# Performance work log

Hardware: AMD Instinct MI355X
Metric: run time of the kernel (lower is better)

Reference implementation:

```python
import jax, jax.numpy as jnp
import numpy as np

B, H, N, D, A = 96, 100, 128, 768, 256  # batch, max_history_num, news_num, news_embedding_dim, attention_dim


def setup_inputs() -> dict:
    key = jax.random.key(0)
    ks = jax.random.split(key, 6)
    w = lambda k, shape: jax.random.normal(k, shape, jnp.float32) * 0.02
    return {
        "history_embedding": jax.random.normal(ks[0], (B, H, D), jnp.float32),
        "candidate_news_representation": jax.random.normal(ks[1], (B, N, D), jnp.float32),
        "W_l": w(ks[2], (D, D)),              # SAGEConv lin_l (neighbor) weight
        "b_l": jnp.zeros((D,), jnp.float32),  # SAGEConv lin_l bias
        "W_r": w(ks[3], (D, D)),              # SAGEConv lin_r (root) weight, bias=False
        "W_K": w(ks[4], (A, D)),              # K Linear, bias=False
        "W_Q": w(ks[5], (A, D)),              # Q Linear, bias=True
        "b_Q": jnp.zeros((A,), jnp.float32),
    }


def reference(history_embedding, candidate_news_representation, W_l, b_l, W_r, W_K, W_Q, b_Q):
    b, h, d = history_embedding.shape
    n = candidate_news_representation.shape[1]
    a_dim = W_K.shape[0]

    # --- GraphSAGE (1 layer SAGEConv, mean aggr, PyG node_dim=-2) ---
    # edge_index: src = user rows 0..b-1 (indexing the history dim!), dst = 0..h-1.
    # Every dst h receives all srcs 0..b-1, so the mean-aggregated neighbor feature is
    # mean over the first b history slots, identical for every h.
    neigh = jnp.mean(history_embedding[:, :b, :], axis=1)  # [b, d]
    gcn = (
        jnp.einsum("bhd,ed->bhe", history_embedding, W_r)
        + (neigh @ W_l.T + b_l)[:, None, :]
    )  # [b, h, d]

    # --- K/Q attention pooling over history ---
    user_rep = gcn[:, 0, :]                                  # [b, d] (gcn_feature[:, :1, :])
    K = jnp.einsum("bhd,ad->bha", gcn, W_K)                  # [b, h, A]
    Q = user_rep @ W_Q.T + b_Q                               # [b, A]
    scores = jnp.einsum("bha,ba->bh", K, Q) / jnp.sqrt(jnp.float32(a_dim))
    alpha = jax.nn.softmax(scores, axis=1)                   # [b, h]
    out = jnp.einsum("bh,bhd->bd", alpha, gcn)               # [b, d]

    # In torch, news_rep/user_rep2 are expand()ed over news_num with identical content,
    # so the per-candidate outputs are all equal: broadcast instead of recomputing.
    return jnp.broadcast_to(out[:, None, :], (b, n, d))
```

## Files before the change

kernel.cpp:

```cpp
#include <hip/hip_runtime.h>
#include <hip/hip_bf16.h>

#define BB 96
#define HH 100
#define NN 128
#define DD 768
#define AA 256

#define WSLAB 196608
#define WSLAB4 49152

static __device__ __forceinline__ float dot4(float4 a, float4 b) {
  return a.x * b.x + a.y * b.y + a.z * b.z + a.w * b.w;
}

__global__ void __launch_bounds__(256)
k_prep(const float* __restrict__ Wr, const float* __restrict__ WK,
       const float* __restrict__ hist,
       float* __restrict__ MTp, float* __restrict__ neighp) {
  int bid = blockIdx.x, tid = threadIdx.x;
  if (bid < 768) {
    __shared__ float sL[32][33];
    __shared__ float sR[32][33];
    int s = bid / 192;
    int t = bid % 192;
    int d0 = (t % 24) * 32, a0 = (t / 24) * 32;
    int tx = tid & 31, ty = tid >> 5;
    float acc[4] = {0.f, 0.f, 0.f, 0.f};
    int ebase = s * 192;
    for (int e0 = ebase; e0 < ebase + 192; e0 += 32) {
#pragma unroll
      for (int k = 0; k < 4; ++k) {
        sL[ty + 8 * k][tx] = WK[(size_t)(a0 + ty + 8 * k) * DD + e0 + tx];
        sR[ty + 8 * k][tx] = Wr[(size_t)(e0 + ty + 8 * k) * DD + d0 + tx];
      }
      __syncthreads();
#pragma unroll 8
      for (int e = 0; e < 32; ++e) {
        float w = sR[e][tx];
#pragma unroll
        for (int k = 0; k < 4; ++k) acc[k] += sL[ty + 8 * k][e] * w;
      }
      __syncthreads();
    }
#pragma unroll
    for (int k = 0; k < 4; ++k) sL[ty + 8 * k][tx] = acc[k];
    __syncthreads();
    float* MTs = MTp + (size_t)s * WSLAB;
#pragma unroll
    for (int k = 0; k < 4; ++k)
      MTs[(size_t)(d0 + ty + 8 * k) * AA + a0 + tx] = sL[tx][ty + 8 * k];
  } else {
    int id = bid - 768;
    int b = id % BB, hg = id / BB;
    if (tid < 192) {
      const float* hb = hist + (size_t)b * HH * DD + (size_t)hg * 12 * DD + tid * 4;
      float4 acc = make_float4(0.f, 0.f, 0.f, 0.f);
#pragma unroll
      for (int i = 0; i < 12; ++i) {
        float4 x = *(const float4*)(hb + (size_t)i * DD);
        acc.x += x.x; acc.y += x.y; acc.z += x.z; acc.w += x.w;
      }
      *(float4*)(neighp + ((size_t)hg * BB + b) * DD + tid * 4) = acc;
    }
  }
}

__global__ void k_nl_u0(const float* __restrict__ neighp, const float* __restrict__ hist,
                        const float* __restrict__ Wl, const float* __restrict__ bl,
                        const float* __restrict__ Wr,
                        float* __restrict__ nl, float* __restrict__ u0) {
  int e0 = blockIdx.x * 32;
  int b0 = blockIdx.y * 3;
  int lane = threadIdx.x & 63, wave = threadIdx.x >> 6;
  float4 xn[3][3], xh[3][3];
#pragma unroll
  for (int bi = 0; bi < 3; ++bi) {
    int b = b0 + bi;
#pragma unroll
    for (int jj = 0; jj < 3; ++jj) {
      int idx = lane + 64 * jj;
      float4 s = make_float4(0.f, 0.f, 0.f, 0.f);
#pragma unroll
      for (int g = 0; g < 8; ++g) {
        float4 x = ((const float4*)(neighp + ((size_t)g * BB + b) * DD))[idx];
        s.x += x.x; s.y += x.y; s.z += x.z; s.w += x.w;
      }
      xn[bi][jj] = make_float4(s.x * (1.f / 96.f), s.y * (1.f / 96.f),
                               s.z * (1.f / 96.f), s.w * (1.f / 96.f));
      xh[bi][jj] = ((const float4*)(hist + (size_t)b * HH * DD))[idx];
    }
  }
  for (int i = 0; i < 8; ++i) {
    int e = e0 + wave * 8 + i;
    const float4* wl4 = (const float4*)(Wl + (size_t)e * DD);
    const float4* wr4 = (const float4*)(Wr + (size_t)e * DD);
    float pl[3] = {0.f, 0.f, 0.f}, pr[3] = {0.f, 0.f, 0.f};
#pragma unroll
    for (int jj = 0; jj < 3; ++jj) {
      float4 wl = wl4[lane + 64 * jj];
      float4 wr = wr4[lane + 64 * jj];
#pragma unroll
      for (int bi = 0; bi < 3; ++bi) {
        pl[bi] += dot4(wl, xn[bi][jj]);
        pr[bi] += dot4(wr, xh[bi][jj]);
      }
    }
#pragma unroll
    for (int bi = 0; bi < 3; ++bi) {
      float pp = pl[bi], qq = pr[bi];
      for (int off = 32; off; off >>= 1) {
        pp += __shfl_down(pp, off, 64);
        qq += __shfl_down(qq, off, 64);
      }
      if (lane == 0) {
        float nle = pp + bl[e];
        nl[(size_t)(b0 + bi) * DD + e] = nle;
        u0[(size_t)(b0 + bi) * DD + e] = qq + nle;
      }
    }
  }
}

__global__ void __launch_bounds__(256)
k_q(const float* __restrict__ u0, const float* __restrict__ WQ,
    const float* __restrict__ bQ, const float* __restrict__ MTp,
    float* __restrict__ Qm, float* __restrict__ MT) {
  int bid = blockIdx.x, tid = threadIdx.x;
  if (bid < 256) {
    int a0 = (bid & 7) * 32;
    int b0 = (bid >> 3) * 3;
    int lane = tid & 63, wave = tid >> 6;
    float4 x[3][3];
#pragma unroll
    for (int bi = 0; bi < 3; ++bi)
#pragma unroll
      for (int jj = 0; jj < 3; ++jj)
        x[bi][jj] = ((const float4*)(u0 + (size_t)(b0 + bi) * DD))[lane + 64 * jj];
    for (int i = 0; i < 8; ++i) {
      int a = a0 + wave * 8 + i;
      const float4* w4 = (const float4*)(WQ + (size_t)a * DD);
      float p[3] = {0.f, 0.f, 0.f};
#pragma unroll
      for (int jj = 0; jj < 3; ++jj) {
        float4 w = w4[lane + 64 * jj];
#pragma unroll
        for (int bi = 0; bi < 3; ++bi) p[bi] += dot4(w, x[bi][jj]);
      }
#pragma unroll
      for (int bi = 0; bi < 3; ++bi) {
        float pp = p[bi];
        for (int off = 32; off; off >>= 1) pp += __shfl_down(pp, off, 64);
        if (lane == 0) Qm[(size_t)(b0 + bi) * AA + a] = pp + bQ[a];
      }
    }
  } else {
    int i4 = (bid - 256) * 256 + tid;
    const float4* p = (const float4*)MTp;
    float4 a = p[i4], b = p[WSLAB4 + i4], c = p[2 * WSLAB4 + i4], d = p[3 * WSLAB4 + i4];
    ((float4*)MT)[i4] = make_float4(a.x + b.x + c.x + d.x, a.y + b.y + c.y + d.y,
                                    a.z + b.z + c.z + d.z, a.w + b.w + c.w + d.w);
  }
}

__global__ void k_v(const float* __restrict__ Qm, const float* __restrict__ MT,
                    float* __restrict__ vv) {
  int d0 = blockIdx.x * 32;
  int b0 = blockIdx.y * 3;
  int lane = threadIdx.x & 63, wave = threadIdx.x >> 6;
  float4 x[3];
#pragma unroll
  for (int bi = 0; bi < 3; ++bi)
    x[bi] = ((const float4*)(Qm + (size_t)(b0 + bi) * AA))[lane];
  for (int i = 0; i < 8; ++i) {
    int d = d0 + wave * 8 + i;
    float4 w = ((const float4*)(MT + (size_t)d * AA))[lane];
    float p[3];
#pragma unroll
    for (int bi = 0; bi < 3; ++bi) p[bi] = dot4(w, x[bi]);
#pragma unroll
    for (int bi = 0; bi < 3; ++bi) {
      float pp = p[bi];
      for (int off = 32; off; off >>= 1) pp += __shfl_down(pp, off, 64);
      if (lane == 0) vv[(size_t)(b0 + bi) * DD + d] = pp * (1.f / 16.f);
    }
  }
}

__global__ void __launch_bounds__(256)
k_attn(const float* __restrict__ hist, const float* __restrict__ vv,
       float* __restrict__ wsum) {
  int b = blockIdx.x;
  int es = blockIdx.y;
  int tid = threadIdx.x, lane = tid & 63, wave = tid >> 6;
  __shared__ __align__(16) float sv[DD];
  __shared__ float sal[HH];
  if (tid < 192)
    ((float4*)sv)[tid] = ((const float4*)(vv + (size_t)b * DD))[tid];
  __syncthreads();
  {
    float4 v0 = ((const float4*)sv)[lane];
    float4 v1 = ((const float4*)sv)[lane + 64];
    float4 v2 = ((const float4*)sv)[lane + 128];
    const float* hb = hist + (size_t)b * HH * DD;
    for (int i = 0; i < 25; ++i) {
      int h = wave * 25 + i;
      const float4* r = (const float4*)(hb + (size_t)h * DD);
      float p = dot4(r[lane], v0) + dot4(r[lane + 64], v1) + dot4(r[lane + 128], v2);
      for (int off = 32; off; off >>= 1) p += __shfl_down(p, off, 64);
      if (lane == 0) sal[h] = p;
    }
  }
  __syncthreads();
  if (wave == 0) {
    float x0 = (lane < HH) ? sal[lane] : -1e30f;
    float x1 = (lane + 64 < HH) ? sal[lane + 64] : -1e30f;
    float m = fmaxf(x0, x1);
    for (int off = 32; off; off >>= 1) m = fmaxf(m, __shfl_xor(m, off, 64));
    float e0 = (lane < HH) ? __expf(x0 - m) : 0.f;
    float e1 = (lane + 64 < HH) ? __expf(x1 - m) : 0.f;
    float s = e0 + e1;
    for (int off = 32; off; off >>= 1) s += __shfl_xor(s, off, 64);
    float inv = 1.f / s;
    if (lane < HH) sal[lane] = e0 * inv;
    if (lane + 64 < HH) sal[lane + 64] = e1 * inv;
  }
  __syncthreads();
  {
    int e = es * 256 + tid;
    const float* hb = hist + (size_t)b * HH * DD + e;
    float acc = 0.f;
    for (int h = 0; h < HH; h += 4) {
      float v0 = hb[(size_t)(h + 0) * DD];
      float v1 = hb[(size_t)(h + 1) * DD];
      float v2 = hb[(size_t)(h + 2) * DD];
      float v3 = hb[(size_t)(h + 3) * DD];
      acc += sal[h + 0] * v0 + sal[h + 1] * v1 + sal[h + 2] * v2 + sal[h + 3] * v3;
    }
    wsum[(size_t)b * DD + e] = acc;
  }
}

__global__ void k_orow_write(const float* __restrict__ wsum, const float* __restrict__ Wr,
                             const float* __restrict__ nl, float* __restrict__ out) {
  int d0 = blockIdx.x * 32;
  int b0 = blockIdx.y * 3;
  int lane = threadIdx.x & 63, wave = threadIdx.x >> 6;
  __shared__ __align__(16) float s_o[3][32];
  float4 x[3][3];
#pragma unroll
  for (int bi = 0; bi < 3; ++bi)
#pragma unroll
    for (int jj = 0; jj < 3; ++jj)
      x[bi][jj] = ((const float4*)(wsum + (size_t)(b0 + bi) * DD))[lane + 64 * jj];
  for (int i = 0; i < 8; ++i) {
    int d = d0 + wave * 8 + i;
    const float4* w4 = (const float4*)(Wr + (size_t)d * DD);
    float p[3] = {0.f, 0.f, 0.f};
#pragma unroll
    for (int jj = 0; jj < 3; ++jj) {
      float4 w = w4[lane + 64 * jj];
#pragma unroll
      for (int bi = 0; bi < 3; ++bi) p[bi] += dot4(w, x[bi][jj]);
    }
#pragma unroll
    for (int bi = 0; bi < 3; ++bi) {
      float pp = p[bi];
      for (int off = 32; off; off >>= 1) pp += __shfl_down(pp, off, 64);
      if (lane == 0)
        s_o[bi][wave * 8 + i] = pp + nl[(size_t)(b0 + bi) * DD + d];
    }
  }
  __syncthreads();
  float4* out4 = (float4*)out;
  int d4 = d0 >> 2;
#pragma unroll
  for (int k = 0; k < 12; ++k) {
    int g = threadIdx.x + (k << 8);
    int seg = g >> 3, off = g & 7;
    int bi = seg >> 7, n = seg & 127;
    float4 val = *(const float4*)&s_o[bi][off * 4];
    out4[((size_t)(b0 + bi) * NN + n) * (DD / 4) + d4 + off] = val;
  }
}

extern "C" void kernel_launch(void* const* d_in, const int* in_sizes, int n_in,
                              void* d_out, int out_size, void* d_ws, size_t ws_size,
                              hipStream_t stream) {
  const float *hist = nullptr, *Wl = nullptr, *Wr = nullptr, *WK = nullptr,
              *WQ = nullptr, *bl = nullptr, *bQ = nullptr;
  int seenDxD = 0, seenAxD = 0;
  for (int i = 0; i < n_in; ++i) {
    int s = in_sizes[i];
    const float* p = (const float*)d_in[i];
    if (s == BB * HH * DD) hist = p;
    else if (s == BB * NN * DD) {  }
    else if (s == DD * DD) { if (seenDxD++ == 0) Wl = p; else Wr = p; }
    else if (s == AA * DD) { if (seenAxD++ == 0) WK = p; else WQ = p; }
    else if (s == DD) bl = p;
    else if (s == AA) bQ = p;
  }

  float* ws = (float*)d_ws;
  float* MTp    = ws + 0;
  float* MT     = ws + 786432;
  float* neighp = ws + 983040;
  float* nl     = ws + 1572864;
  float* u0     = ws + 1646592;
  float* Qm     = ws + 1720320;
  float* vv     = ws + 1744896;
  float* wsum   = ws + 1818624;
  float* out = (float*)d_out;

  k_prep      <<<dim3(1536),   dim3(256), 0, stream>>>(Wr, WK, hist, MTp, neighp);
  k_nl_u0     <<<dim3(24, 32), dim3(256), 0, stream>>>(neighp, hist, Wl, bl, Wr, nl, u0);
  k_q         <<<dim3(448),    dim3(256), 0, stream>>>(u0, WQ, bQ, MTp, Qm, MT);
  k_v         <<<dim3(24, 32), dim3(256), 0, stream>>>(Qm, MT, vv);
  k_attn      <<<dim3(96, 3),  dim3(256), 0, stream>>>(hist, vv, wsum);
  k_orow_write<<<dim3(24, 32), dim3(256), 0, stream>>>(wsum, Wr, nl, out);
}
```

Baseline: 99.22 us.

## Split attention into separate score and weighted-sum kernels with more blocks

The fused attention kernel is split in two. A score kernel computes the history-vector dot products over 96x5 blocks. A weighted-sum kernel then reads the scores, applies the softmax, and splits both the embedding dimension and the history range across waves, reducing the partial sums through shared memory. Separately, the neighbor partial-sum step now sums 24 rows per block with two accumulators instead of 12 rows, so it needs fewer blocks and fewer partials. This exposes more parallelism for the memory-bound attention pass, at the cost of an extra launch and extra reads of the history tensor.

```diff
diff --git a/kernel.cpp b/kernel.cpp
--- a/kernel.cpp
+++ b/kernel.cpp
@@ -54,14 +54,18 @@
     int id = bid - 768;
     int b = id % BB, hg = id / BB;
     if (tid < 192) {
-      const float* hb = hist + (size_t)b * HH * DD + (size_t)hg * 12 * DD + tid * 4;
-      float4 acc = make_float4(0.f, 0.f, 0.f, 0.f);
-#pragma unroll
-      for (int i = 0; i < 12; ++i) {
-        float4 x = *(const float4*)(hb + (size_t)i * DD);
-        acc.x += x.x; acc.y += x.y; acc.z += x.z; acc.w += x.w;
-      }
-      *(float4*)(neighp + ((size_t)hg * BB + b) * DD + tid * 4) = acc;
+      const float* hb = hist + (size_t)b * HH * DD + (size_t)hg * 24 * DD + tid * 4;
+      float4 a0 = make_float4(0.f, 0.f, 0.f, 0.f);
+      float4 a1 = make_float4(0.f, 0.f, 0.f, 0.f);
+#pragma unroll
+      for (int h = 0; h < 24; h += 2) {
+        float4 x = *(const float4*)(hb + (size_t)h * DD);
+        float4 y = *(const float4*)(hb + (size_t)(h + 1) * DD);
+        a0.x += x.x; a0.y += x.y; a0.z += x.z; a0.w += x.w;
+        a1.x += y.x; a1.y += y.y; a1.z += y.z; a1.w += y.w;
+      }
+      float4 m = make_float4(a0.x + a1.x, a0.y + a1.y, a0.z + a1.z, a0.w + a1.w);
+      *(float4*)(neighp + ((size_t)hg * BB + b) * DD + tid * 4) = m;
     }
   }
 }
@@ -82,7 +86,7 @@
       int idx = lane + 64 * jj;
       float4 s = make_float4(0.f, 0.f, 0.f, 0.f);
 #pragma unroll
-      for (int g = 0; g < 8; ++g) {
+      for (int g = 0; g < 4; ++g) {
         float4 x = ((const float4*)(neighp + ((size_t)g * BB + b) * DD))[idx];
         s.x += x.x; s.y += x.y; s.z += x.z; s.w += x.w;
       }
@@ -187,30 +191,35 @@
   }
 }
 
+__global__ void k_scores(const float* __restrict__ hist, const float* __restrict__ vv,
+                         float* __restrict__ sc) {
+  int b = blockIdx.x, hg = blockIdx.y;
+  int lane = threadIdx.x & 63, wave = threadIdx.x >> 6;
+  float4 v[3];
+  const float4* vb = (const float4*)(vv + (size_t)b * DD);
+#pragma unroll
+  for (int jj = 0; jj < 3; ++jj) v[jj] = vb[lane + 64 * jj];
+  const float* hb = hist + (size_t)b * HH * DD;
+  for (int i = 0; i < 5; ++i) {
+    int h = hg * 20 + wave * 5 + i;
+    const float4* r = (const float4*)(hb + (size_t)h * DD);
+    float p = 0.f;
+#pragma unroll
+    for (int jj = 0; jj < 3; ++jj) p += dot4(r[lane + 64 * jj], v[jj]);
+    for (int off = 32; off; off >>= 1) p += __shfl_down(p, off, 64);
+    if (lane == 0) sc[b * 128 + h] = p;
+  }
+}
+
 __global__ void __launch_bounds__(256)
-k_attn(const float* __restrict__ hist, const float* __restrict__ vv,
+k_wsum(const float* __restrict__ hist, const float* __restrict__ sc,
        float* __restrict__ wsum) {
   int b = blockIdx.x;
   int es = blockIdx.y;
   int tid = threadIdx.x, lane = tid & 63, wave = tid >> 6;
-  __shared__ __align__(16) float sv[DD];
   __shared__ float sal[HH];
-  if (tid < 192)
-    ((float4*)sv)[tid] = ((const float4*)(vv + (size_t)b * DD))[tid];
-  __syncthreads();
-  {
-    float4 v0 = ((const float4*)sv)[lane];
-    float4 v1 = ((const float4*)sv)[lane + 64];
-    float4 v2 = ((const float4*)sv)[lane + 128];
-    const float* hb = hist + (size_t)b * HH * DD;
-    for (int i = 0; i < 25; ++i) {
-      int h = wave * 25 + i;
-      const float4* r = (const float4*)(hb + (size_t)h * DD);
-      float p = dot4(r[lane], v0) + dot4(r[lane + 64], v1) + dot4(r[lane + 128], v2);
-      for (int off = 32; off; off >>= 1) p += __shfl_down(p, off, 64);
-      if (lane == 0) sal[h] = p;
-    }
-  }
+  __shared__ float psum[4][64];
+  if (tid < HH) sal[tid] = sc[b * 128 + tid];
   __syncthreads();
   if (wave == 0) {
     float x0 = (lane < HH) ? sal[lane] : -1e30f;
@@ -226,18 +235,25 @@
     if (lane + 64 < HH) sal[lane + 64] = e1 * inv;
   }
   __syncthreads();
-  {
-    int e = es * 256 + tid;
-    const float* hb = hist + (size_t)b * HH * DD + e;
-    float acc = 0.f;
-    for (int h = 0; h < HH; h += 4) {
-      float v0 = hb[(size_t)(h + 0) * DD];
-      float v1 = hb[(size_t)(h + 1) * DD];
-      float v2 = hb[(size_t)(h + 2) * DD];
-      float v3 = hb[(size_t)(h + 3) * DD];
-      acc += sal[h + 0] * v0 + sal[h + 1] * v1 + sal[h + 2] * v2 + sal[h + 3] * v3;
-    }
-    wsum[(size_t)b * DD + e] = acc;
+  int e = es * 64 + lane;
+  const float* hb = hist + (size_t)b * HH * DD + e;
+  int h0 = wave * 25;
+  float acc = 0.f;
+#pragma unroll
+  for (int i = 0; i < 25; i += 5) {
+    float v0 = hb[(size_t)(h0 + i + 0) * DD];
+    float v1 = hb[(size_t)(h0 + i + 1) * DD];
+    float v2 = hb[(size_t)(h0 + i + 2) * DD];
+    float v3 = hb[(size_t)(h0 + i + 3) * DD];
+    float v4 = hb[(size_t)(h0 + i + 4) * DD];
+    acc += sal[h0 + i + 0] * v0 + sal[h0 + i + 1] * v1 + sal[h0 + i + 2] * v2 +
+           sal[h0 + i + 3] * v3 + sal[h0 + i + 4] * v4;
+  }
+  psum[wave][lane] = acc;
+  __syncthreads();
+  if (tid < 64) {
+    float s = psum[0][tid] + psum[1][tid] + psum[2][tid] + psum[3][tid];
+    wsum[(size_t)b * DD + es * 64 + tid] = s;
   }
 }
 
@@ -305,17 +321,19 @@
   float* MTp    = ws + 0;
   float* MT     = ws + 786432;
   float* neighp = ws + 983040;
-  float* nl     = ws + 1572864;
-  float* u0     = ws + 1646592;
-  float* Qm     = ws + 1720320;
-  float* vv     = ws + 1744896;
-  float* wsum   = ws + 1818624;
+  float* nl     = ws + 1277952;
+  float* u0     = ws + 1351680;
+  float* Qm     = ws + 1425408;
+  float* vv     = ws + 1449984;
+  float* sc     = ws + 1523712;
+  float* wsum   = ws + 1536000;
   float* out = (float*)d_out;
 
-  k_prep      <<<dim3(1536),   dim3(256), 0, stream>>>(Wr, WK, hist, MTp, neighp);
+  k_prep      <<<dim3(1152),   dim3(256), 0, stream>>>(Wr, WK, hist, MTp, neighp);
   k_nl_u0     <<<dim3(24, 32), dim3(256), 0, stream>>>(neighp, hist, Wl, bl, Wr, nl, u0);
   k_q         <<<dim3(448),    dim3(256), 0, stream>>>(u0, WQ, bQ, MTp, Qm, MT);
   k_v         <<<dim3(24, 32), dim3(256), 0, stream>>>(Qm, MT, vv);
-  k_attn      <<<dim3(96, 3),  dim3(256), 0, stream>>>(hist, vv, wsum);
+  k_scores    <<<dim3(96, 5),  dim3(256), 0, stream>>>(hist, vv, sc);
+  k_wsum      <<<dim3(96, 12), dim3(256), 0, stream>>>(hist, sc, wsum);
   k_orow_write<<<dim3(24, 32), dim3(256), 0, stream>>>(wsum, Wr, nl, out);
 }
```

Result: faster. 87.43 us (median of 2 runs) (-11.9%).
